# Performance work log

Measured on AMD Instinct MI355X. Metric: run time of the kernel, lower is better.

Reference implementation:

```python
import jax, jax.numpy as jnp
import numpy as np

N, IN_DIM, H1, D, K, E, HEADS = 4096, 3000, 512, 64, 32, 49152, 4
ATT_THRESH = 0.25


def setup_inputs() -> dict:
    key = jax.random.key(0)
    ks = jax.random.split(key, 20)
    glorot = lambda k, fi, fo: jax.random.normal(k, (fi, fo), jnp.float32) * (2.0 / (fi + fo)) ** 0.5
    return {
        "x": jax.random.normal(ks[0], (N, IN_DIM), jnp.float32),
        "edge_index": jax.random.randint(ks[1], (2, E), 0, N, jnp.int32),
        "sub_nodes": jax.random.randint(ks[2], (N, K), 0, N, jnp.int32),
        # GCN encoder: in_dim -> 512 -> 64
        "enc_w1": glorot(ks[3], IN_DIM, H1), "enc_b1": jnp.zeros((H1,), jnp.float32),
        "enc_w2": glorot(ks[4], H1, D), "enc_b2": jnp.zeros((D,), jnp.float32),
        # linear decoder: 64 -> 512 -> in_dim
        "dec_w1": glorot(ks[5], D, H1), "dec_b1": jnp.zeros((H1,), jnp.float32),
        "dec_w2": glorot(ks[6], H1, IN_DIM), "dec_b2": jnp.zeros((IN_DIM,), jnp.float32),
        # MultiheadAttention (torch layout: in_proj_weight [3D, D], out_proj.weight [D, D])
        "attn_in_w": jax.random.normal(ks[7], (3 * D, D), jnp.float32) * (2.0 / D) ** 0.5,
        "attn_in_b": jnp.zeros((3 * D,), jnp.float32),
        "attn_out_w": jax.random.normal(ks[8], (D, D), jnp.float32) * (2.0 / D) ** 0.5,
        "attn_out_b": jnp.zeros((D,), jnp.float32),
        # Bilinear discriminator
        "bil_w": glorot(ks[9], D, D), "bil_b": jnp.zeros((), jnp.float32),
    }


def _gcn_conv(x, src, dst, W, b):
    n = x.shape[0]
    deg = jax.ops.segment_sum(jnp.ones(src.shape, x.dtype), dst, num_segments=n) + 1.0
    inv = jax.lax.rsqrt(deg)
    h = x @ W  # [n, out]
    coef = (inv[src] * inv[dst])[:, None]
    agg = jax.ops.segment_sum(h[src] * coef, dst, num_segments=n)
    agg = agg + h * (inv * inv)[:, None]  # self-loop contribution
    return agg + b


def _mha(x, in_w, in_b, out_w, out_b):
    # x: [N, D]; torch MultiheadAttention with batch of 1, dropout=0
    n, d = x.shape
    dh = d // HEADS
    qkv = x @ in_w.T + in_b  # [N, 3D]
    q, k, v = jnp.split(qkv, 3, axis=-1)
    rs = lambda t: t.reshape(n, HEADS, dh).transpose(1, 0, 2)  # [H, N, dh]
    q, k, v = rs(q), rs(k), rs(v)
    scores = jnp.einsum("hnd,hmd->hnm", q, k) / jnp.sqrt(jnp.asarray(dh, x.dtype))
    attn = jax.nn.softmax(scores, axis=-1)  # [H, N, N]
    out = jnp.einsum("hnm,hmd->hnd", attn, v).transpose(1, 0, 2).reshape(n, d)
    out = out @ out_w.T + out_b
    return out, attn.mean(axis=0)  # averaged attn weights [N, N]


def reference(x, edge_index, sub_nodes,
              enc_w1, enc_b1, enc_w2, enc_b2,
              dec_w1, dec_b1, dec_w2, dec_b2,
              attn_in_w, attn_in_b, attn_out_w, attn_out_b,
              bil_w, bil_b):
    src, dst = edge_index[0], edge_index[1]
    # GCN encoder
    h = jax.nn.relu(_gcn_conv(x, src, dst, enc_w1, enc_b1))
    spot_emb = _gcn_conv(h, src, dst, enc_w2, enc_b2)  # [N, D]
    # per-node subgraph gather + mean pool (global_mean_pool over fixed-size niches)
    local_niches = spot_emb[sub_nodes].mean(axis=1)  # [N, D]
    # linear decoder
    recon = jax.nn.relu(local_niches @ dec_w1 + dec_b1) @ dec_w2 + dec_b2
    # self-attention over all spots
    global_niches, attn_w = _mha(local_niches, attn_in_w, attn_in_b, attn_out_w, attn_out_b)
    # low-attention negative sampling
    n = local_niches.shape[0]
    kk = int(n * ATT_THRESH)
    _, idx = jax.lax.top_k(-attn_w, kk)  # smallest-k per row
    rand_idx = jax.random.randint(jax.random.key(42), (n,), 0, kk)
    sampled = idx[jnp.arange(n), rand_idx]
    neg_global = global_niches[sampled]
    # bilinear discriminator logits
    logits_pos = jnp.einsum("nd,de,ne->n", local_niches, bil_w, global_niches) + bil_b
    logits_neg = jnp.einsum("nd,de,ne->n", local_niches, bil_w, neg_global) + bil_b
    return recon, logits_pos, logits_neg
```

## Files before the change

### kernel.cpp

```cpp
#include <hip/hip_runtime.h>
#include <hip/hip_bf16.h>
#include <stdint.h>

#define NN      4096
#define INDIM   3000
#define H1DIM   512
#define DDIM    64
#define RECON_ELEMS (NN * INDIM)

typedef __attribute__((ext_vector_type(8))) __bf16          bf16x8;
typedef __attribute__((ext_vector_type(8))) unsigned short  u16x8;
typedef __attribute__((ext_vector_type(4))) float           f32x4;
typedef __attribute__((ext_vector_type(4))) unsigned int    u32x4;

__device__ __forceinline__ unsigned short f2bf(float f) {
  union { float f; unsigned int i; } v; v.f = f;
  unsigned int x = v.i;
  unsigned int lsb = (x >> 16) & 1u;
  x += 0x7FFFu + lsb;
  return (unsigned short)(x >> 16);
}

__device__ __forceinline__ void tf2x32(unsigned k0, unsigned k1, unsigned x0, unsigned x1,
                                       unsigned &o0, unsigned &o1) {
  unsigned ks2 = k0 ^ k1 ^ 0x1BD11BDAu;
  x0 += k0; x1 += k1;
#define TFR(r) { x0 += x1; x1 = (x1 << (r)) | (x1 >> (32 - (r))); x1 ^= x0; }
  TFR(13) TFR(15) TFR(26) TFR(6)
  x0 += k1; x1 += ks2 + 1u;
  TFR(17) TFR(29) TFR(16) TFR(24)
  x0 += ks2; x1 += k0 + 2u;
  TFR(13) TFR(15) TFR(26) TFR(6)
  x0 += k0; x1 += k1 + 3u;
  TFR(17) TFR(29) TFR(16) TFR(24)
  x0 += k1; x1 += ks2 + 4u;
  TFR(13) TFR(15) TFR(26) TFR(6)
  x0 += ks2; x1 += k0 + 5u;
#undef TFR
  o0 = x0; o1 = x1;
}

__global__ void k_deg(const int* __restrict__ dst, int* __restrict__ cnt, int E) {
  int e = blockIdx.x * 256 + threadIdx.x;
  if (e < E) atomicAdd(&cnt[dst[e]], 1);
}

__global__ void k_inv(const int* __restrict__ cnt, float* __restrict__ inv) {
  int n = blockIdx.x * 256 + threadIdx.x;
  if (n < NN) inv[n] = 1.0f / sqrtf((float)cnt[n] + 1.0f);
}

__global__ __launch_bounds__(1024) void k_scan(const int* __restrict__ cnt, int* __restrict__ offs) {
  __shared__ int ssum[1024];
  int tid = threadIdx.x;
  int c0 = cnt[tid*4], c1 = cnt[tid*4+1], c2 = cnt[tid*4+2], c3 = cnt[tid*4+3];
  int s = c0 + c1 + c2 + c3;
  ssum[tid] = s;
  __syncthreads();
  for (int off = 1; off < 1024; off <<= 1) {
    int v = (tid >= off) ? ssum[tid - off] : 0;
    __syncthreads();
    ssum[tid] += v;
    __syncthreads();
  }
  int base = ssum[tid] - s;
  offs[tid*4]   = base;
  offs[tid*4+1] = base + c0;
  offs[tid*4+2] = base + c0 + c1;
  offs[tid*4+3] = base + c0 + c1 + c2;
  if (tid == 1023) offs[4096] = ssum[1023];
}

__global__ void k_scatter(const int* __restrict__ dst, const int* __restrict__ offs,
                          int* __restrict__ cur, int* __restrict__ eid, int E) {
  int e = blockIdx.x * 256 + threadIdx.x;
  if (e < E) {
    int d = dst[e];
    int pos = offs[d] + atomicAdd(&cur[d], 1);
    eid[pos] = e;
  }
}

__global__ void k_sort(const int* __restrict__ offs, int* __restrict__ eid) {
  int n = blockIdx.x * 256 + threadIdx.x;
  if (n >= NN) return;
  int b = offs[n], e = offs[n+1];
  for (int i = b + 1; i < e; i++) {
    int v = eid[i]; int j = i - 1;
    while (j >= b && eid[j] > v) { eid[j+1] = eid[j]; j--; }
    eid[j+1] = v;
  }
}

#define FBK 16
__global__ __launch_bounds__(256) void k_gemm_f32(
    const float* __restrict__ A, const float* __restrict__ B, float* __restrict__ C) {
  __shared__ float As[2][FBK * 132];
  __shared__ float Bs[2][FBK * 132];
  const int tid = threadIdx.x;
  const int m0 = blockIdx.y * 128;
  const int n0 = blockIdx.x * 128;
  const int z  = blockIdx.z;
  const int kBeg = z ? 1504 : 0;
  const int kEnd = z ? 3000 : 1504;
  C += (size_t)z * NN * 512;
  const int lane = tid & 63, w = tid >> 6;
  const int rg = w * 4 + (lane >> 4);
  const int cg = lane & 15;
  f32x4 acc[2][2][4];
#pragma unroll
  for (int a = 0; a < 2; a++)
#pragma unroll
    for (int b = 0; b < 2; b++)
#pragma unroll
      for (int i = 0; i < 4; i++) acc[a][b][i] = (f32x4){0.f,0.f,0.f,0.f};

  const int arow = tid & 127;
  const int asl  = tid >> 7;
  const int bkr  = tid >> 4;
  const int bcq  = tid & 15;

  f32x4 ra[2], rb0, rb1;
  {
    const int kt = kBeg;
    const bool full = (kt + FBK <= kEnd);
#pragma unroll
    for (int it = 0; it < 2; it++) {
      int kk = (asl * 2 + it) * 4;
      if (full) {
        ra[it] = *(const f32x4*)(A + (size_t)(m0 + arow) * INDIM + kt + kk);
      } else {
#pragma unroll
        for (int j = 0; j < 4; j++)
          ra[it][j] = (kt + kk + j < kEnd) ? A[(size_t)(m0 + arow) * INDIM + kt + kk + j] : 0.f;
      }
    }
    if (full || kt + bkr < kEnd) {
      const float* bp = B + (size_t)(kt + bkr) * 512 + n0 + bcq * 8;
      rb0 = *(const f32x4*)bp;
      rb1 = *(const f32x4*)(bp + 4);
    } else { rb0 = (f32x4){0.f,0.f,0.f,0.f}; rb1 = rb0; }
  }

  int buf = 0;
  for (int kt = kBeg; kt < kEnd; kt += FBK) {
#pragma unroll
    for (int it = 0; it < 2; it++) {
      int kk = (asl * 2 + it) * 4;
      As[buf][(kk+0)*132 + arow] = ra[it][0];
      As[buf][(kk+1)*132 + arow] = ra[it][1];
      As[buf][(kk+2)*132 + arow] = ra[it][2];
      As[buf][(kk+3)*132 + arow] = ra[it][3];
    }
    *(f32x4*)&Bs[buf][bkr*132 + bcq*8]     = rb0;
    *(f32x4*)&Bs[buf][bkr*132 + bcq*8 + 4] = rb1;
    __syncthreads();
    const int ktn = kt + FBK;
    if (ktn < kEnd) {
      const bool fulln = (ktn + FBK <= kEnd);
#pragma unroll
      for (int it = 0; it < 2; it++) {
        int kk = (asl * 2 + it) * 4;
        if (fulln) {
          ra[it] = *(const f32x4*)(A + (size_t)(m0 + arow) * INDIM + ktn + kk);
        } else {
#pragma unroll
          for (int j = 0; j < 4; j++)
            ra[it][j] = (ktn + kk + j < kEnd) ? A[(size_t)(m0 + arow) * INDIM + ktn + kk + j] : 0.f;
        }
      }
      if (fulln || ktn + bkr < kEnd) {
        const float* bp = B + (size_t)(ktn + bkr) * 512 + n0 + bcq * 8;
        rb0 = *(const f32x4*)bp;
        rb1 = *(const f32x4*)(bp + 4);
      } else { rb0 = (f32x4){0.f,0.f,0.f,0.f}; rb1 = rb0; }
    }
    const float* Asb = As[buf];
    const float* Bsb = Bs[buf];
#pragma unroll
    for (int k = 0; k < FBK; k++) {
      f32x4 a0 = *(const f32x4*)&Asb[k*132 + rg*4];
      f32x4 a1 = *(const f32x4*)&Asb[k*132 + 64 + rg*4];
      f32x4 b0 = *(const f32x4*)&Bsb[k*132 + cg*4];
      f32x4 b1 = *(const f32x4*)&Bsb[k*132 + 64 + cg*4];
#pragma unroll
      for (int i = 0; i < 4; i++)
#pragma unroll
        for (int j = 0; j < 4; j++) {
          acc[0][0][i][j] = fmaf(a0[i], b0[j], acc[0][0][i][j]);
          acc[0][1][i][j] = fmaf(a0[i], b1[j], acc[0][1][i][j]);
          acc[1][0][i][j] = fmaf(a1[i], b0[j], acc[1][0][i][j]);
          acc[1][1][i][j] = fmaf(a1[i], b1[j], acc[1][1][i][j]);
        }
    }
    buf ^= 1;
  }
#pragma unroll
  for (int a = 0; a < 2; a++)
#pragma unroll
    for (int i = 0; i < 4; i++) {
      int gr = m0 + a*64 + rg*4 + i;
#pragma unroll
      for (int b = 0; b < 2; b++)
        *(f32x4*)(C + (size_t)gr * 512 + n0 + b*64 + cg*4) = acc[a][b][i];
    }
}

__global__ void k_combine(float* __restrict__ c0, const float* __restrict__ c1) {
  int i = blockIdx.x * 256 + threadIdx.x;
  ((f32x4*)c0)[i] = ((const f32x4*)c0)[i] + ((const f32x4*)c1)[i];
}

__global__ __launch_bounds__(256) void k_gemm_bf(
    const unsigned short* __restrict__ A, const float* __restrict__ B,
    float* __restrict__ Cf, unsigned short* __restrict__ Cb,
    const float* __restrict__ bias,
    int M, int N, int K, int ldc, int mode) {
  __shared__ __attribute__((aligned(16))) unsigned short As[128 * 40];
  __shared__ __attribute__((aligned(16))) unsigned short Bs[128 * 40];
  const int tid  = threadIdx.x;
  const int m0   = blockIdx.y * 128;
  const int n0   = blockIdx.x * 128;
  const int lane = tid & 63;
  const int wid  = tid >> 6;
  const int wm   = wid >> 1, wn = wid & 1;
  const int lrow = lane & 15, lk = lane >> 4;

  f32x4 acc[4][4];
#pragma unroll
  for (int i = 0; i < 4; i++)
#pragma unroll
    for (int j = 0; j < 4; j++) acc[i][j] = (f32x4){0.f, 0.f, 0.f, 0.f};

  for (int k0 = 0; k0 < K; k0 += 32) {
#pragma unroll
    for (int it = 0; it < 2; it++) {
      int c   = it * 256 + tid;
      int row = c >> 2, kc = c & 3;
      int kg  = k0 + kc * 8;
      u16x8 v = *(const u16x8*)(A + (size_t)(m0 + row) * K + kg);
      *(u16x8*)&As[row * 40 + kc * 8] = v;
    }
    {
      int kk_ = tid & 31;
      int nc0 = tid >> 5;
      int kg  = k0 + kk_;
#pragma unroll
      for (int it = 0; it < 2; it++) {
        int nc = nc0 + it * 8;
        int ng = n0 + nc * 8;
        unsigned short vb[8];
        if (ng + 8 <= N) {
          f32x4 f0 = *(const f32x4*)(B + (size_t)kg * N + ng);
          f32x4 f1 = *(const f32x4*)(B + (size_t)kg * N + ng + 4);
#pragma unroll
          for (int j = 0; j < 4; j++) { vb[j] = f2bf(f0[j]); vb[4+j] = f2bf(f1[j]); }
        } else {
#pragma unroll
          for (int j = 0; j < 8; j++)
            vb[j] = (ng + j < N) ? f2bf(B[(size_t)kg * N + ng + j]) : (unsigned short)0;
        }
#pragma unroll
        for (int j = 0; j < 8; j++) Bs[(nc * 8 + j) * 40 + kk_] = vb[j];
      }
    }
    __syncthreads();
    bf16x8 af[4], bfr[4];
#pragma unroll
    for (int mi = 0; mi < 4; mi++) {
      u16x8 r = *(const u16x8*)&As[(wm * 64 + mi * 16 + lrow) * 40 + lk * 8];
      af[mi] = __builtin_bit_cast(bf16x8, r);
    }
#pragma unroll
    for (int ni = 0; ni < 4; ni++) {
      u16x8 r = *(const u16x8*)&Bs[(wn * 64 + ni * 16 + lrow) * 40 + lk * 8];
      bfr[ni] = __builtin_bit_cast(bf16x8, r);
    }
#pragma unroll
    for (int mi = 0; mi < 4; mi++)
#pragma unroll
      for (int ni = 0; ni < 4; ni++)
        acc[mi][ni] = __builtin_amdgcn_mfma_f32_16x16x32_bf16(af[mi], bfr[ni], acc[mi][ni], 0, 0, 0);
    __syncthreads();
  }

#pragma unroll
  for (int mi = 0; mi < 4; mi++)
#pragma unroll
    for (int ni = 0; ni < 4; ni++)
#pragma unroll
      for (int reg = 0; reg < 4; reg++) {
        int gr = m0 + wm * 64 + mi * 16 + lk * 4 + reg;
        int gc = n0 + wn * 64 + ni * 16 + lrow;
        if (gc < N) {
          float v = acc[mi][ni][reg] + bias[gc];
          if (mode == 1) {
            if (v < 0.f) v = 0.f;
            Cb[(size_t)gr * ldc + gc] = f2bf(v);
          } else {
            Cf[(size_t)gr * ldc + gc] = v;
          }
        }
      }
}

__global__ __launch_bounds__(256) void k_agg(
    const float* __restrict__ X, float* __restrict__ Y,
    const float* __restrict__ bias, const int* __restrict__ offs,
    const int* __restrict__ eid, const int* __restrict__ esrc,
    const float* __restrict__ inv, int F, int relu) {
  int n = blockIdx.x;
  int beg = offs[n], end = offs[n + 1];
  float invn = inv[n];
  float inv2 = invn * invn;
  for (int d = threadIdx.x; d < F; d += 256) {
    float acc = 0.f;
    for (int t = beg; t < end; t++) {
      int e = eid[t]; int s = esrc[e];
      float cf = inv[s] * invn;
      acc += X[(size_t)s * F + d] * cf;
    }
    acc += X[(size_t)n * F + d] * inv2;
    acc += bias[d];
    if (relu && acc < 0.f) acc = 0.f;
    Y[(size_t)n * F + d] = acc;
  }
}

__global__ __launch_bounds__(256) void k_mmw2(const float* __restrict__ h,
                                              const float* __restrict__ w2,
                                              float* __restrict__ out) {
  __shared__ float hs[4 * 512];
  int tid  = threadIdx.x;
  int brow = blockIdx.x * 4;
  const f32x4* src = (const f32x4*)(h + (size_t)brow * 512);
  f32x4* dst4 = (f32x4*)hs;
  dst4[tid]       = src[tid];
  dst4[tid + 256] = src[tid + 256];
  __syncthreads();
  int r = tid >> 6, c = tid & 63;
  float acc = 0.f;
  const float* hr = hs + r * 512;
#pragma unroll 8
  for (int k = 0; k < 512; k++) acc = fmaf(hr[k], w2[k * 64 + c], acc);
  out[(size_t)(brow + r) * 64 + c] = acc;
}

__global__ void k_pool(const float* __restrict__ spot, const int* __restrict__ sub,
                       float* __restrict__ local, unsigned short* __restrict__ local_bf) {
  int n = blockIdx.x, d = threadIdx.x;
  float acc = 0.f;
  for (int j = 0; j < 32; j++) {
    int s = sub[n * 32 + j];
    acc += spot[(size_t)s * 64 + d];
  }
  float lv = acc * 0.03125f;
  local[(size_t)n * 64 + d] = lv;
  local_bf[(size_t)n * 64 + d] = f2bf(lv);
}

__global__ void k_qkv(const float* __restrict__ local, const float* __restrict__ iw,
                      const float* __restrict__ ib,
                      float* __restrict__ Qp, float* __restrict__ Kp, float* __restrict__ Vp) {
  __shared__ float lx[64];
  int n = blockIdx.x, t = threadIdx.x;
  if (t < 64) lx[t] = local[(size_t)n * 64 + t];
  __syncthreads();
  float acc = 0.f;
#pragma unroll 8
  for (int d = 0; d < 64; d++) acc = fmaf(lx[d], iw[t * 64 + d], acc);
  acc += ib[t];
  if (t < 64)       Qp[(size_t)n * 64 + t] = acc;
  else if (t < 128) Kp[(size_t)n * 64 + (t - 64)] = acc;
  else              Vp[(size_t)n * 64 + (t - 128)] = acc;
}

#define RT 2
__global__ __launch_bounds__(256, 3) void k_attn(
    const float* __restrict__ Qp, const float* __restrict__ Kp, const float* __restrict__ Vp,
    float* __restrict__ ctx, int* __restrict__ sampled) {
  __shared__ __attribute__((aligned(16))) float regA[2][64 * 64];
  __shared__ float sMZ[2][2][4];
  __shared__ unsigned wtot[4];
  __shared__ unsigned sh_prefix;
  __shared__ int sh_r;

  const int t   = threadIdx.x;
  const int n0  = blockIdx.x * RT;
  const int sm  = t & 63;
  const int sq  = (t >> 6) & 1;
  const int shp = t >> 7;
  const int dq  = t & 15;
  const int me  = t >> 4;
  const int stm = t >> 4;
  const int stc = t & 15;
  const int wv  = t >> 6;
  const int lane = t & 63;

  float Qreg[32];
  {
    const float* qp = Qp + (size_t)(n0 + sq) * 64 + shp * 32;
#pragma unroll
    for (int j = 0; j < 8; j++) {
      f32x4 qv = *(const f32x4*)(qp + j * 4);
      Qreg[j * 4 + 0] = qv[0]; Qreg[j * 4 + 1] = qv[1];
      Qreg[j * 4 + 2] = qv[2]; Qreg[j * 4 + 3] = qv[3];
    }
  }

  const int hsel = stc >> 2;
  const int rr   = stc & 3;
  float qsh[2][4];
#pragma unroll
  for (int q = 0; q < 2; q++) {
    f32x4 qv = *(const f32x4*)(Qp + (size_t)(n0 + q) * 64 + stc * 4);
    qsh[q][0] = qv[0]; qsh[q][1] = qv[1]; qsh[q][2] = qv[2]; qsh[q][3] = qv[3];
  }

  float M[2] = {-3.0e38f, -3.0e38f}, Z[2] = {0.f, 0.f};
  {
    f32x4 ka[4], kb[4];
#pragma unroll
    for (int j = 0; j < 4; j++) {
      ka[j] = *(const f32x4*)(Kp + (size_t)(j * 16 + stm) * 64 + stc * 4);
      kb[j] = *(const f32x4*)(Kp + (size_t)(64 + j * 16 + stm) * 64 + stc * 4);
    }
    for (int tp = 0; tp < 64; tp += 2) {
#pragma unroll
      for (int half = 0; half < 2; half++) {
        f32x4 k0 = (half == 0) ? ka[0] : kb[0];
        f32x4 k1 = (half == 0) ? ka[1] : kb[1];
        f32x4 k2 = (half == 0) ? ka[2] : kb[2];
        f32x4 k3 = (half == 0) ? ka[3] : kb[3];
        float s00 = 0.f, s01 = 0.f, s02 = 0.f, s03 = 0.f;
        float s10 = 0.f, s11 = 0.f, s12 = 0.f, s13 = 0.f;
#pragma unroll
        for (int e = 0; e < 4; e++) {
          s00 = fmaf(qsh[0][e], k0[e], s00);
          s01 = fmaf(qsh[0][e], k1[e], s01);
          s02 = fmaf(qsh[0][e], k2[e], s02);
          s03 = fmaf(qsh[0][e], k3[e], s03);
          s10 = fmaf(qsh[1][e], k0[e], s10);
          s11 = fmaf(qsh[1][e], k1[e], s11);
          s12 = fmaf(qsh[1][e], k2[e], s12);
          s13 = fmaf(qsh[1][e], k3[e], s13);
        }
        if (tp + 2 + half < 64) {
#pragma unroll
          for (int j = 0; j < 4; j++) {
            f32x4 v = *(const f32x4*)(Kp + (size_t)((tp + 2 + half) * 64 + j * 16 + stm) * 64 + stc * 4);
            if (half == 0) ka[j] = v; else kb[j] = v;
          }
        }
        s00 += __shfl_xor(s00, 1, 64); s00 += __shfl_xor(s00, 2, 64);
        s01 += __shfl_xor(s01, 1, 64); s01 += __shfl_xor(s01, 2, 64);
        s02 += __shfl_xor(s02, 1, 64); s02 += __shfl_xor(s02, 2, 64);
        s03 += __shfl_xor(s03, 1, 64); s03 += __shfl_xor(s03, 2, 64);
        s10 += __shfl_xor(s10, 1, 64); s10 += __shfl_xor(s10, 2, 64);
        s11 += __shfl_xor(s11, 1, 64); s11 += __shfl_xor(s11, 2, 64);
        s12 += __shfl_xor(s12, 1, 64); s12 += __shfl_xor(s12, 2, 64);
        s13 += __shfl_xor(s13, 1, 64); s13 += __shfl_xor(s13, 2, 64);
        float sv0 = (rr == 0) ? s00 : (rr == 1) ? s01 : (rr == 2) ? s02 : s03;
        float sv1 = (rr == 0) ? s10 : (rr == 1) ? s11 : (rr == 2) ? s12 : s13;
        sv0 *= 0.25f; sv1 *= 0.25f;
        if (sv0 > M[0]) { Z[0] = fmaf(Z[0], __expf(M[0] - sv0), 1.0f); M[0] = sv0; }
        else            Z[0] += __expf(sv0 - M[0]);
        if (sv1 > M[1]) { Z[1] = fmaf(Z[1], __expf(M[1] - sv1), 1.0f); M[1] = sv1; }
        else            Z[1] += __expf(sv1 - M[1]);
      }
    }
  }
  {
    float* redM = regA[0];
    float* redZ = regA[0] + 512;
    int slot = stm + 16 * rr;
    redM[(0 * 4 + hsel) * 64 + slot] = M[0];
    redM[(1 * 4 + hsel) * 64 + slot] = M[1];
    redZ[(0 * 4 + hsel) * 64 + slot] = Z[0];
    redZ[(1 * 4 + hsel) * 64 + slot] = Z[1];
    __syncthreads();
    if (t < 8) {
      const float* pm = &redM[t * 64];
      const float* pz = &redZ[t * 64];
      float Mv = -3.0e38f, Zv = 0.f;
      for (int i = 0; i < 64; i++) {
        float m_ = pm[i], z_ = pz[i];
        if (m_ > Mv) { Zv = fmaf(Zv, __expf(Mv - m_), z_); Mv = m_; }
        else         Zv = fmaf(z_, __expf(m_ - Mv), Zv);
      }
      sMZ[0][t >> 2][t & 3] = Mv;
      sMZ[1][t >> 2][t & 3] = Zv;
    }
    __syncthreads();
  }
  float Mh[2], iZ[2];
#pragma unroll
  for (int hh = 0; hh < 2; hh++) {
    Mh[hh] = sMZ[0][sq][shp * 2 + hh];
    iZ[hh] = 1.0f / sMZ[1][sq][shp * 2 + hh];
  }
  __syncthreads();

  f32x4 kA[4];
#pragma unroll
  for (int jj = 0; jj < 4; jj++)
    kA[jj] = *(const f32x4*)(Kp + (size_t)(jj * 16 + stm) * 64 + stc * 4);
  float* KtB   = regA[0];
  float* Pt    = regA[1];
  float* rvbuf = regA[1] + 1024;
  float o4[2][4];
#pragma unroll
  for (int q = 0; q < 2; q++)
#pragma unroll
    for (int e = 0; e < 4; e++) o4[q][e] = 0.f;
  float rv[2][16];

  for (int sb = 0; sb < 4; sb++) {
    for (int ti = 0; ti < 16; ti++) {
      const int tile = sb * 16 + ti;
#pragma unroll
      for (int jj = 0; jj < 4; jj++) {
        int m = jj * 16 + stm;
        int sc = (stc + (m & 15) + 4 * (m >> 4)) & 15;
        *(f32x4*)&KtB[(m * 16 + sc) * 4] = kA[jj];
      }
      __syncthreads();
      if (tile + 1 < 64) {
#pragma unroll
        for (int jj = 0; jj < 4; jj++)
          kA[jj] = *(const f32x4*)(Kp + (size_t)((tile + 1) * 64 + jj * 16 + stm) * 64 + stc * 4);
      }
      {
        float s[2] = {0.f, 0.f};
#pragma unroll
        for (int ci = 0; ci < 8; ci++) {
          int c = shp * 8 + ci;
          int sc = (c + (sm & 15) + 4 * (sm >> 4)) & 15;
          f32x4 k4 = *(const f32x4*)&KtB[(sm * 16 + sc) * 4];
          int hh = ci >> 2;
#pragma unroll
          for (int e = 0; e < 4; e++)
            s[hh] = fmaf(Qreg[ci * 4 + e], k4[e], s[hh]);
        }
#pragma unroll
        for (int hh = 0; hh < 2; hh++) {
          float p = __expf(s[hh] * 0.25f - Mh[hh]) * iZ[hh];
          Pt[(sq * 4 + shp * 2 + hh) * 68 + sm] = p;
        }
      }
      f32x4 vt[4];
#pragma unroll
      for (int i = 0; i < 4; i++)
        vt[i] = *(const f32x4*)(Vp + (size_t)(tile * 64 + me * 4 + i) * 64 + dq * 4);
      __syncthreads();
      if (wv == sb) {
        rvbuf[(0 * 16 + ti) * 64 + lane] =
            0.25f * (Pt[0 * 68 + lane] + Pt[1 * 68 + lane] +
                     Pt[2 * 68 + lane] + Pt[3 * 68 + lane]);
        rvbuf[(1 * 16 + ti) * 64 + lane] =
            0.25f * (Pt[4 * 68 + lane] + Pt[5 * 68 + lane] +
                     Pt[6 * 68 + lane] + Pt[7 * 68 + lane]);
      }
      {
        int h = dq >> 2;
        f32x4 p4[2];
#pragma unroll
        for (int q = 0; q < 2; q++)
          p4[q] = *(const f32x4*)&Pt[(q * 4 + h) * 68 + me * 4];
#pragma unroll
        for (int i = 0; i < 4; i++) {
#pragma unroll
          for (int q = 0; q < 2; q++)
#pragma unroll
            for (int e = 0; e < 4; e++)
              o4[q][e] = fmaf(p4[q][i], vt[i][e], o4[q][e]);
        }
      }
    }
    if (wv == sb) {
#pragma unroll
      for (int g = 0; g < 16; g++) {
        rv[0][g] = rvbuf[(0 * 16 + g) * 64 + lane];
        rv[1][g] = rvbuf[(1 * 16 + g) * 64 + lane];
      }
    }
  }

  {
    float* Osh = regA[0];
#pragma unroll
    for (int q = 0; q < 2; q++)
#pragma unroll
      for (int e = 0; e < 4; e++)
        Osh[((me * 2 + q) * 16 + dq) * 4 + e] = o4[q][e];
    __syncthreads();
    if (t < 128) {
      int q2 = t >> 6, d = t & 63;
      float acc = 0.f;
      for (int i = 0; i < 16; i++)
        acc += Osh[((i * 2 + q2) * 16 + (d >> 2)) * 4 + (d & 3)];
      ctx[(size_t)(n0 + q2) * 64 + d] = acc;
    }
    __syncthreads();
  }

  unsigned* histT = (unsigned*)regA[0];
  unsigned* gaux  = ((unsigned*)regA[0]) + 1024;
#pragma unroll
  for (int q = 0; q < RT; q++) {
    int n = n0 + q;
    if (t == 0) {
      unsigned a0, a1, b0, b1;
      tf2x32(0u, 42u, 0u, 2u, a0, a1);
      tf2x32(0u, 42u, 1u, 3u, b0, b1);
      unsigned o0, o1, bits;
      if (n < 2048) { tf2x32(a1, b1, (unsigned)n, (unsigned)(n + 2048), o0, o1); bits = o0; }
      else          { tf2x32(a1, b1, (unsigned)(n - 2048), (unsigned)n, o0, o1); bits = o1; }
      sh_r = (int)(bits & 1023u);
      sh_prefix = 0u;
    }
    __syncthreads();
    int r = sh_r;
    unsigned prefix = 0u;
    for (int level = 0; level < 4; level++) {
      int shift = 24 - 8 * level;
      unsigned c0 = 0, c1 = 0, c2 = 0, c3 = 0;
#pragma unroll
      for (int g = 0; g < 16; g++) {
        unsigned u = __float_as_uint(rv[q][g]);
        bool ok = (level == 0) || ((u >> (shift + 8)) == (prefix >> (shift + 8)));
        unsigned bin = (u >> shift) & 255u;
        unsigned long long mok = __ballot(ok);
        unsigned long long b0 = __ballot(bin & 1u);
        unsigned long long b1 = __ballot(bin & 2u);
        unsigned long long b2 = __ballot(bin & 4u);
        unsigned long long b3 = __ballot(bin & 8u);
        unsigned long long b4 = __ballot(bin & 16u);
        unsigned long long b5 = __ballot(bin & 32u);
        unsigned long long b6 = __ballot(bin & 64u);
        unsigned long long b7 = __ballot(bin & 128u);
        unsigned long long m = mok;
        m &= (lane & 1)  ? b0 : ~b0;
        m &= (lane & 2)  ? b1 : ~b1;
        m &= (lane & 4)  ? b2 : ~b2;
        m &= (lane & 8)  ? b3 : ~b3;
        m &= (lane & 16) ? b4 : ~b4;
        m &= (lane & 32) ? b5 : ~b5;
        c0 += (unsigned)__builtin_popcountll(m & ~b6 & ~b7);
        c1 += (unsigned)__builtin_popcountll(m &  b6 & ~b7);
        c2 += (unsigned)__builtin_popcountll(m & ~b6 &  b7);
        c3 += (unsigned)__builtin_popcountll(m &  b6 &  b7);
      }
      histT[wv * 256 + lane]       = c0;
      histT[wv * 256 + 64 + lane]  = c1;
      histT[wv * 256 + 128 + lane] = c2;
      histT[wv * 256 + 192 + lane] = c3;
      __syncthreads();
      unsigned own = histT[t] + histT[256 + t] + histT[512 + t] + histT[768 + t];
      unsigned v = own;
      for (int off = 1; off < 64; off <<= 1) {
        unsigned u2 = __shfl_up(v, off, 64);
        if ((t & 63) >= off) v += u2;
      }
      if ((t & 63) == 63) wtot[t >> 6] = v;
      __syncthreads();
      unsigned basev = 0;
#pragma unroll
      for (int w = 0; w < 4; w++) if (w < (t >> 6)) basev += wtot[w];
      v += basev;
      unsigned cb = v - own;
      if ((unsigned)r >= cb && (unsigned)r < v) {
        sh_prefix = prefix | ((unsigned)t << shift);
        sh_r = r - (int)cb;
      }
      __syncthreads();
      prefix = sh_prefix; r = sh_r;
    }
    {
      unsigned long long msk[16];
#pragma unroll
      for (int g = 0; g < 16; g++)
        msk[g] = __ballot(__float_as_uint(rv[q][g]) == prefix);
      if (lane == 0) {
#pragma unroll
        for (int g = 0; g < 16; g++)
          gaux[wv * 16 + g] = (unsigned)__builtin_popcountll(msk[g]);
      }
      __syncthreads();
      if (t < 64) {
        unsigned acc = 0;
        for (int i = 0; i < t; i++) acc += gaux[i];
        gaux[64 + t] = acc;
      }
      __syncthreads();
#pragma unroll
      for (int g = 0; g < 16; g++) {
        if (__float_as_uint(rv[q][g]) == prefix) {
          unsigned before = (unsigned)__builtin_popcountll(msk[g] & ((1ull << lane) - 1ull));
          if ((int)(gaux[64 + wv * 16 + g] + before) == r)
            sampled[n] = (wv * 16 + g) * 64 + lane;
        }
      }
      __syncthreads();
    }
  }
}

__global__ void k_outproj(const float* __restrict__ ctx, const float* __restrict__ ow,
                          const float* __restrict__ ob, float* __restrict__ gni) {
  __shared__ float cx[64];
  int n = blockIdx.x, t = threadIdx.x;
  cx[t] = ctx[(size_t)n * 64 + t];
  __syncthreads();
  float acc = 0.f;
#pragma unroll 8
  for (int j = 0; j < 64; j++) acc = fmaf(cx[j], ow[t * 64 + j], acc);
  gni[(size_t)n * 64 + t] = acc + ob[t];
}

__global__ void k_logits(const float* __restrict__ local, const float* __restrict__ gni,
                         const int* __restrict__ sampled,
                         const float* __restrict__ bw, const float* __restrict__ bb,
                         float* __restrict__ outp, float* __restrict__ outn) {
  __shared__ float lv[64], gp[64], gn[64];
  int n = blockIdx.x, t = threadIdx.x;
  int sm = sampled[n];
  lv[t] = local[(size_t)n * 64 + t];
  gp[t] = gni[(size_t)n * 64 + t];
  gn[t] = gni[(size_t)sm * 64 + t];
  __syncthreads();
  float tp = 0.f, tn = 0.f;
#pragma unroll 8
  for (int e = 0; e < 64; e++) {
    float w = bw[t * 64 + e];
    tp = fmaf(w, gp[e], tp);
    tn = fmaf(w, gn[e], tn);
  }
  float vp = lv[t] * tp, vn = lv[t] * tn;
  for (int off = 32; off; off >>= 1) {
    vp += __shfl_down(vp, off, 64);
    vn += __shfl_down(vn, off, 64);
  }
  if (t == 0) {
    outp[n] = vp + bb[0];
    outn[n] = vn + bb[0];
  }
}

extern "C" void kernel_launch(void* const* d_in, const int* in_sizes, int n_in,
                              void* d_out, int out_size, void* d_ws, size_t ws_size,
                              hipStream_t stream) {
  const float* x      = (const float*)d_in[0];
  const int*   edge   = (const int*)d_in[1];
  const int*   sub    = (const int*)d_in[2];
  const float* enc_w1 = (const float*)d_in[3];
  const float* enc_b1 = (const float*)d_in[4];
  const float* enc_w2 = (const float*)d_in[5];
  const float* enc_b2 = (const float*)d_in[6];
  const float* dec_w1 = (const float*)d_in[7];
  const float* dec_b1 = (const float*)d_in[8];
  const float* dec_w2 = (const float*)d_in[9];
  const float* dec_b2 = (const float*)d_in[10];
  const float* ain_w  = (const float*)d_in[11];
  const float* ain_b  = (const float*)d_in[12];
  const float* aout_w = (const float*)d_in[13];
  const float* aout_b = (const float*)d_in[14];
  const float* bil_w  = (const float*)d_in[15];
  const float* bil_b  = (const float*)d_in[16];
  float* out = (float*)d_out;

  const int E = in_sizes[1] / 2;
  const int* esrc = edge;
  const int* edst = edge + E;

  char* base = (char*)d_ws;
  const size_t MB = (size_t)1 << 20;
  float*          cpart    = (float*)(base + 0);
  float*          h_pre    = (float*)(base + 0);
  unsigned short* dech_bf  = (unsigned short*)(base + 0);
  float*          h        = (float*)(base + 8*MB);
  float*          Qp       = (float*)(base + 8*MB);
  float*          Kp       = (float*)(base + 9*MB);
  float*          Vp       = (float*)(base + 10*MB);
  float*          ctx      = (float*)(base + 11*MB);
  float*          gni      = (float*)(base + 12*MB);
  float*          hw2      = (float*)(base + 16*MB);
  float*          spot     = (float*)(base + 17*MB);
  float*          localf   = (float*)(base + 18*MB);
  unsigned short* local_bf = (unsigned short*)(base + 19*MB);
  char* ip = base + 19*MB + 512*1024;
  float* inv    = (float*)ip;  ip += 16384;
  int*   degcnt = (int*)ip;    ip += 16384;
  int*   cursor = (int*)ip;    ip += 16384;
  int*   offs   = (int*)ip;    ip += 16640;
  int*   sampled= (int*)ip;    ip += 16384;
  int*   eid    = (int*)ip;    ip += (size_t)E * 4;

  hipMemsetAsync(degcnt, 0, (size_t)NN * 4, stream);
  hipMemsetAsync(cursor, 0, (size_t)NN * 4, stream);

  int egrid = (E + 255) / 256;
  k_deg<<<egrid, 256, 0, stream>>>(edst, degcnt, E);
  k_inv<<<(NN + 255) / 256, 256, 0, stream>>>(degcnt, inv);
  k_scan<<<1, 1024, 0, stream>>>(degcnt, offs);
  k_scatter<<<egrid, 256, 0, stream>>>(edst, offs, cursor, eid, E);
  k_sort<<<(NN + 255) / 256, 256, 0, stream>>>(offs, eid);

  {
    dim3 g(4, 32, 2);
    k_gemm_f32<<<g, 256, 0, stream>>>(x, enc_w1, cpart);
  }
  k_combine<<<(NN * 512 / 4) / 256, 256, 0, stream>>>(h_pre, cpart + (size_t)NN * 512);
  k_agg<<<NN, 256, 0, stream>>>(h_pre, h, enc_b1, offs, eid, esrc, inv, 512, 1);
  k_mmw2<<<NN / 4, 256, 0, stream>>>(h, enc_w2, hw2);
  k_agg<<<NN, 256, 0, stream>>>(hw2, spot, enc_b2, offs, eid, esrc, inv, 64, 0);
  k_pool<<<NN, 64, 0, stream>>>(spot, sub, localf, local_bf);

  {
    dim3 g(4, 32);
    k_gemm_bf<<<g, 256, 0, stream>>>(local_bf, dec_w1, nullptr, dech_bf, dec_b1,
                                     NN, 512, 64, 512, 1);
  }
  {
    dim3 g(24, 32);
    k_gemm_bf<<<g, 256, 0, stream>>>(dech_bf, dec_w2, out, nullptr, dec_b2,
                                     NN, INDIM, 512, INDIM, 2);
  }

  k_qkv<<<NN, 192, 0, stream>>>(localf, ain_w, ain_b, Qp, Kp, Vp);
  k_attn<<<NN / RT, 256, 0, stream>>>(Qp, Kp, Vp, ctx, sampled);
  k_outproj<<<NN, 64, 0, stream>>>(ctx, aout_w, aout_b, gni);
  k_logits<<<NN, 64, 0, stream>>>(localf, gni, sampled, bil_w, bil_b,
                                  out + RECON_ELEMS, out + RECON_ELEMS + NN);
}
```

Measured before the change: 921.7 us.

## Restructure attention second pass to reuse first-pass register layout and drop LDS staging

The second attention pass (probabilities times V) now uses the same per-thread key/column layout as the softmax-statistics pass. K is loaded directly into registers with a two-tile prefetch, scores are reduced with lane shuffles, and each thread accumulates a 2x16 output slice straight from global V. This removes the shared-memory K transpose, the P staging buffer and the two barriers per tile that the old path needed. In exchange it uses more registers for the accumulators, V loads are less coalesced, and output reduction across 64 slots moves into a padded shared-memory pass.

```diff
diff --git a/kernel.cpp b/kernel.cpp
--- a/kernel.cpp
+++ b/kernel.cpp
@@ -379,7 +379,8 @@
 __global__ __launch_bounds__(256, 3) void k_attn(
     const float* __restrict__ Qp, const float* __restrict__ Kp, const float* __restrict__ Vp,
     float* __restrict__ ctx, int* __restrict__ sampled) {
-  __shared__ __attribute__((aligned(16))) float regA[2][64 * 64];
+  __shared__ __attribute__((aligned(16))) float smem[256 * 17];
+  __shared__ __attribute__((aligned(16))) float rvS[2 * 16 * 64];
   __shared__ float sMZ[2][2][4];
   __shared__ unsigned wtot[4];
   __shared__ unsigned sh_prefix;
@@ -387,29 +388,13 @@
 
   const int t   = threadIdx.x;
   const int n0  = blockIdx.x * RT;
-  const int sm  = t & 63;
-  const int sq  = (t >> 6) & 1;
-  const int shp = t >> 7;
-  const int dq  = t & 15;
-  const int me  = t >> 4;
   const int stm = t >> 4;
   const int stc = t & 15;
   const int wv  = t >> 6;
   const int lane = t & 63;
-
-  float Qreg[32];
-  {
-    const float* qp = Qp + (size_t)(n0 + sq) * 64 + shp * 32;
-#pragma unroll
-    for (int j = 0; j < 8; j++) {
-      f32x4 qv = *(const f32x4*)(qp + j * 4);
-      Qreg[j * 4 + 0] = qv[0]; Qreg[j * 4 + 1] = qv[1];
-      Qreg[j * 4 + 2] = qv[2]; Qreg[j * 4 + 3] = qv[3];
-    }
-  }
-
   const int hsel = stc >> 2;
   const int rr   = stc & 3;
+
   float qsh[2][4];
 #pragma unroll
   for (int q = 0; q < 2; q++) {
@@ -471,8 +456,8 @@
     }
   }
   {
-    float* redM = regA[0];
-    float* redZ = regA[0] + 512;
+    float* redM = smem;
+    float* redZ = smem + 512;
     int slot = stm + 16 * rr;
     redM[(0 * 4 + hsel) * 64 + slot] = M[0];
     redM[(1 * 4 + hsel) * 64 + slot] = M[1];
@@ -493,119 +478,133 @@
     }
     __syncthreads();
   }
-  float Mh[2], iZ[2];
-#pragma unroll
-  for (int hh = 0; hh < 2; hh++) {
-    Mh[hh] = sMZ[0][sq][shp * 2 + hh];
-    iZ[hh] = 1.0f / sMZ[1][sq][shp * 2 + hh];
-  }
-  __syncthreads();
-
-  f32x4 kA[4];
-#pragma unroll
-  for (int jj = 0; jj < 4; jj++)
-    kA[jj] = *(const f32x4*)(Kp + (size_t)(jj * 16 + stm) * 64 + stc * 4);
-  float* KtB   = regA[0];
-  float* Pt    = regA[1];
-  float* rvbuf = regA[1] + 1024;
-  float o4[2][4];
+  float Mh2[2], iZ2[2];
+#pragma unroll
+  for (int q = 0; q < 2; q++) {
+    Mh2[q] = sMZ[0][q][hsel];
+    iZ2[q] = 1.0f / sMZ[1][q][hsel];
+  }
+
+  float o[2][16];
 #pragma unroll
   for (int q = 0; q < 2; q++)
 #pragma unroll
-    for (int e = 0; e < 4; e++) o4[q][e] = 0.f;
+    for (int d = 0; d < 16; d++) o[q][d] = 0.f;
   float rv[2][16];
 
-  for (int sb = 0; sb < 4; sb++) {
-    for (int ti = 0; ti < 16; ti++) {
-      const int tile = sb * 16 + ti;
-#pragma unroll
-      for (int jj = 0; jj < 4; jj++) {
-        int m = jj * 16 + stm;
-        int sc = (stc + (m & 15) + 4 * (m >> 4)) & 15;
-        *(f32x4*)&KtB[(m * 16 + sc) * 4] = kA[jj];
-      }
-      __syncthreads();
-      if (tile + 1 < 64) {
-#pragma unroll
-        for (int jj = 0; jj < 4; jj++)
-          kA[jj] = *(const f32x4*)(Kp + (size_t)((tile + 1) * 64 + jj * 16 + stm) * 64 + stc * 4);
-      }
-      {
-        float s[2] = {0.f, 0.f};
-#pragma unroll
-        for (int ci = 0; ci < 8; ci++) {
-          int c = shp * 8 + ci;
-          int sc = (c + (sm & 15) + 4 * (sm >> 4)) & 15;
-          f32x4 k4 = *(const f32x4*)&KtB[(sm * 16 + sc) * 4];
-          int hh = ci >> 2;
-#pragma unroll
-          for (int e = 0; e < 4; e++)
-            s[hh] = fmaf(Qreg[ci * 4 + e], k4[e], s[hh]);
+  {
+    f32x4 ka[4], kb[4];
+#pragma unroll
+    for (int j = 0; j < 4; j++) {
+      ka[j] = *(const f32x4*)(Kp + (size_t)(j * 16 + stm) * 64 + stc * 4);
+      kb[j] = *(const f32x4*)(Kp + (size_t)(64 + j * 16 + stm) * 64 + stc * 4);
+    }
+    for (int sb = 0; sb < 4; sb++) {
+      for (int tp = 0; tp < 16; tp += 2) {
+#pragma unroll
+        for (int half = 0; half < 2; half++) {
+          const int ti   = tp + half;
+          const int tile = sb * 16 + ti;
+          f32x4 k0 = (half == 0) ? ka[0] : kb[0];
+          f32x4 k1 = (half == 0) ? ka[1] : kb[1];
+          f32x4 k2 = (half == 0) ? ka[2] : kb[2];
+          f32x4 k3 = (half == 0) ? ka[3] : kb[3];
+          float s00 = 0.f, s01 = 0.f, s02 = 0.f, s03 = 0.f;
+          float s10 = 0.f, s11 = 0.f, s12 = 0.f, s13 = 0.f;
+#pragma unroll
+          for (int e = 0; e < 4; e++) {
+            s00 = fmaf(qsh[0][e], k0[e], s00);
+            s01 = fmaf(qsh[0][e], k1[e], s01);
+            s02 = fmaf(qsh[0][e], k2[e], s02);
+            s03 = fmaf(qsh[0][e], k3[e], s03);
+            s10 = fmaf(qsh[1][e], k0[e], s10);
+            s11 = fmaf(qsh[1][e], k1[e], s11);
+            s12 = fmaf(qsh[1][e], k2[e], s12);
+            s13 = fmaf(qsh[1][e], k3[e], s13);
+          }
+          if (tile + 2 < 64) {
+#pragma unroll
+            for (int j = 0; j < 4; j++) {
+              f32x4 v = *(const f32x4*)(Kp + (size_t)((tile + 2) * 64 + j * 16 + stm) * 64 + stc * 4);
+              if (half == 0) ka[j] = v; else kb[j] = v;
+            }
+          }
+          s00 += __shfl_xor(s00, 1, 64); s00 += __shfl_xor(s00, 2, 64);
+          s01 += __shfl_xor(s01, 1, 64); s01 += __shfl_xor(s01, 2, 64);
+          s02 += __shfl_xor(s02, 1, 64); s02 += __shfl_xor(s02, 2, 64);
+          s03 += __shfl_xor(s03, 1, 64); s03 += __shfl_xor(s03, 2, 64);
+          s10 += __shfl_xor(s10, 1, 64); s10 += __shfl_xor(s10, 2, 64);
+          s11 += __shfl_xor(s11, 1, 64); s11 += __shfl_xor(s11, 2, 64);
+          s12 += __shfl_xor(s12, 1, 64); s12 += __shfl_xor(s12, 2, 64);
+          s13 += __shfl_xor(s13, 1, 64); s13 += __shfl_xor(s13, 2, 64);
+          float sv0 = (rr == 0) ? s00 : (rr == 1) ? s01 : (rr == 2) ? s02 : s03;
+          float sv1 = (rr == 0) ? s10 : (rr == 1) ? s11 : (rr == 2) ? s12 : s13;
+          float p0 = __expf(sv0 * 0.25f - Mh2[0]) * iZ2[0];
+          float p1 = __expf(sv1 * 0.25f - Mh2[1]) * iZ2[1];
+          int lbase = lane & 48;
+          int lrr   = lane & 3;
+          float g01 = __shfl(p0, lbase | (4 + lrr), 64);
+          float g02 = __shfl(p0, lbase | (8 + lrr), 64);
+          float g03 = __shfl(p0, lbase | (12 + lrr), 64);
+          float g11 = __shfl(p1, lbase | (4 + lrr), 64);
+          float g12 = __shfl(p1, lbase | (8 + lrr), 64);
+          float g13 = __shfl(p1, lbase | (12 + lrr), 64);
+          if (hsel == 0) {
+            int slot = stm + 16 * rr;
+            rvS[(0 * 16 + ti) * 64 + slot] = 0.25f * (((p0 + g01) + g02) + g03);
+            rvS[(1 * 16 + ti) * 64 + slot] = 0.25f * (((p1 + g11) + g12) + g13);
+          }
+          {
+            const float* vp = Vp + (size_t)(tile * 64 + stm + 16 * rr) * 64 + hsel * 16;
+            f32x4 v0 = *(const f32x4*)(vp);
+            f32x4 v1 = *(const f32x4*)(vp + 4);
+            f32x4 v2 = *(const f32x4*)(vp + 8);
+            f32x4 v3 = *(const f32x4*)(vp + 12);
+#pragma unroll
+            for (int e = 0; e < 4; e++) {
+              o[0][e]      = fmaf(p0, v0[e], o[0][e]);
+              o[0][4 + e]  = fmaf(p0, v1[e], o[0][4 + e]);
+              o[0][8 + e]  = fmaf(p0, v2[e], o[0][8 + e]);
+              o[0][12 + e] = fmaf(p0, v3[e], o[0][12 + e]);
+              o[1][e]      = fmaf(p1, v0[e], o[1][e]);
+              o[1][4 + e]  = fmaf(p1, v1[e], o[1][4 + e]);
+              o[1][8 + e]  = fmaf(p1, v2[e], o[1][8 + e]);
+              o[1][12 + e] = fmaf(p1, v3[e], o[1][12 + e]);
+            }
+          }
         }
-#pragma unroll
-        for (int hh = 0; hh < 2; hh++) {
-          float p = __expf(s[hh] * 0.25f - Mh[hh]) * iZ[hh];
-          Pt[(sq * 4 + shp * 2 + hh) * 68 + sm] = p;
-        }
-      }
-      f32x4 vt[4];
-#pragma unroll
-      for (int i = 0; i < 4; i++)
-        vt[i] = *(const f32x4*)(Vp + (size_t)(tile * 64 + me * 4 + i) * 64 + dq * 4);
+      }
       __syncthreads();
       if (wv == sb) {
-        rvbuf[(0 * 16 + ti) * 64 + lane] =
-            0.25f * (Pt[0 * 68 + lane] + Pt[1 * 68 + lane] +
-                     Pt[2 * 68 + lane] + Pt[3 * 68 + lane]);
-        rvbuf[(1 * 16 + ti) * 64 + lane] =
-            0.25f * (Pt[4 * 68 + lane] + Pt[5 * 68 + lane] +
-                     Pt[6 * 68 + lane] + Pt[7 * 68 + lane]);
-      }
-      {
-        int h = dq >> 2;
-        f32x4 p4[2];
-#pragma unroll
-        for (int q = 0; q < 2; q++)
-          p4[q] = *(const f32x4*)&Pt[(q * 4 + h) * 68 + me * 4];
-#pragma unroll
-        for (int i = 0; i < 4; i++) {
-#pragma unroll
-          for (int q = 0; q < 2; q++)
-#pragma unroll
-            for (int e = 0; e < 4; e++)
-              o4[q][e] = fmaf(p4[q][i], vt[i][e], o4[q][e]);
+#pragma unroll
+        for (int g = 0; g < 16; g++) {
+          rv[0][g] = rvS[(0 * 16 + g) * 64 + lane];
+          rv[1][g] = rvS[(1 * 16 + g) * 64 + lane];
         }
       }
-    }
-    if (wv == sb) {
-#pragma unroll
-      for (int g = 0; g < 16; g++) {
-        rv[0][g] = rvbuf[(0 * 16 + g) * 64 + lane];
-        rv[1][g] = rvbuf[(1 * 16 + g) * 64 + lane];
-      }
-    }
-  }
-
-  {
-    float* Osh = regA[0];
-#pragma unroll
-    for (int q = 0; q < 2; q++)
-#pragma unroll
-      for (int e = 0; e < 4; e++)
-        Osh[((me * 2 + q) * 16 + dq) * 4 + e] = o4[q][e];
-    __syncthreads();
-    if (t < 128) {
-      int q2 = t >> 6, d = t & 63;
+      __syncthreads();
+    }
+  }
+
+#pragma unroll
+  for (int q = 0; q < 2; q++) {
+#pragma unroll
+    for (int d = 0; d < 16; d++) smem[t * 17 + d] = o[q][d];
+    __syncthreads();
+    if (t < 64) {
+      int hh = t >> 4, d = t & 15;
       float acc = 0.f;
-      for (int i = 0; i < 16; i++)
-        acc += Osh[((i * 2 + q2) * 16 + (d >> 2)) * 4 + (d & 3)];
-      ctx[(size_t)(n0 + q2) * 64 + d] = acc;
-    }
-    __syncthreads();
-  }
-
-  unsigned* histT = (unsigned*)regA[0];
-  unsigned* gaux  = ((unsigned*)regA[0]) + 1024;
+      for (int s = 0; s < 64; s++) {
+        int to = (s & 15) * 16 + hh * 4 + (s >> 4);
+        acc += smem[to * 17 + d];
+      }
+      ctx[(size_t)(n0 + q) * 64 + t] = acc;
+    }
+    __syncthreads();
+  }
+
+  unsigned* histT = (unsigned*)smem;
+  unsigned* gaux  = ((unsigned*)smem) + 1024;
 #pragma unroll
   for (int q = 0; q < RT; q++) {
     int n = n0 + q;
```

Result: slower. 983.1 us (+6.7%).
